# Performance work log

Hardware: AMD Instinct MI355X
Metric: run time of the kernel (lower is better)

The kernel has to match this reference:

```python
import jax, jax.numpy as jnp
import numpy as np

N_NODES = 100000
E_RAW = 3200000
IN_CH = 256
HID = 128
OUT = 64
N_LAYERS = 4


def setup_inputs() -> dict:
    rng = np.random.default_rng(0)
    src = rng.integers(0, N_NODES, E_RAW)
    dst = rng.integers(0, N_NODES, E_RAW)
    # drop self loops (add_self_loops appends them explicitly) and dedupe so the
    # edge list is coalesced (torch sparse .pow acts on coalesced values)
    code = src.astype(np.int64) * N_NODES + dst.astype(np.int64)
    code = np.unique(code[src != dst])
    edge_index = jnp.asarray(np.stack([code // N_NODES, code % N_NODES]), dtype=jnp.int32)

    key = jax.random.key(0)
    ks = jax.random.split(key, 6)
    stdv = 1.0 / np.sqrt(HID)
    x = jax.random.normal(ks[0], (N_NODES, IN_CH), jnp.float32)
    W_lin1 = jax.random.uniform(ks[1], (IN_CH, HID), jnp.float32, -stdv, stdv)
    b_lin1 = jnp.zeros((HID,), jnp.float32)
    W1 = jax.random.uniform(ks[2], (N_LAYERS, HID, HID), jnp.float32, -stdv, stdv)
    W2 = jax.random.uniform(ks[3], (N_LAYERS, HID, HID), jnp.float32, -stdv, stdv)
    W_lin2 = jax.random.uniform(ks[4], (HID, OUT), jnp.float32, -stdv, stdv)
    b_lin2 = jnp.zeros((OUT,), jnp.float32)
    return {"x": x, "W_lin1": W_lin1, "b_lin1": b_lin1, "W1": W1, "W2": W2,
            "W_lin2": W_lin2, "b_lin2": b_lin2, "edge_index": edge_index}


def reference(x, W_lin1, b_lin1, W1, W2, W_lin2, b_lin2, edge_index):
    n = N_NODES
    diag = jnp.arange(n, dtype=edge_index.dtype)
    # add self loops (appended last, so diagonal entries are the final n slots)
    row = jnp.concatenate([edge_index[0], diag])
    col = jnp.concatenate([edge_index[1], diag])
    deg = jax.ops.segment_sum(jnp.ones_like(row, jnp.float32), row, num_segments=n)
    inv_deg_row = 1.0 / deg[row]                     # per-edge 1/deg(src)
    a_vals = inv_deg_row                             # A_rw = D^{-1} A (incl. self loops)
    l_vals = (-inv_deg_row).at[-n:].add(1.0)         # L_rw = I - D^{-1} A (coalesced)

    def spmm(vals, X):
        return jax.ops.segment_sum(vals[:, None] * X[col], row, num_segments=n)

    h = jax.nn.relu(x @ W_lin1 + b_lin1)
    acc = jnp.zeros((n, HID), h.dtype)
    for l in range(N_LAYERS):
        o1 = h @ W1[l]
        o2 = h @ W2[l]
        if l != 0:
            # torch sparse .pow(l) = elementwise power of nonzero values
            o1 = spmm(l_vals ** l, o1)
            o2 = spmm(a_vals ** l, o2)
        if l != N_LAYERS - 1:
            o1 = spmm(a_vals, o1)
            o2 = spmm(l_vals, o2)
        acc = acc + jax.nn.relu(o1) + jax.nn.relu(o2)
    xm = acc / (2 * N_LAYERS)
    return xm @ W_lin2 + b_lin2
```

## Files before the change

kernel.cpp:

```cpp
#include <hip/hip_runtime.h>
#include <hip/hip_bf16.h>
#include <stdint.h>

#define NN   100000
#define ICH  256
#define HID  128
#define OUTF 64

typedef float  f32x4  __attribute__((ext_vector_type(4)));
typedef __bf16 bf16x8 __attribute__((ext_vector_type(8)));

__device__ __forceinline__ float bf2f(uint16_t u){
  union { uint32_t i; float f; } v; v.i = ((uint32_t)u) << 16; return v.f;
}
__device__ __forceinline__ uint16_t f2bf(float f){
  union { float f; uint32_t i; } v; v.f = f;
  uint32_t i = v.i;
  return (uint16_t)((i + 0x7FFFu + ((i >> 16) & 1u)) >> 16);
}
__device__ __forceinline__ uint32_t pack2(float a, float b){
  return (uint32_t)f2bf(a) | ((uint32_t)f2bf(b) << 16);
}

__global__ void k_csr(const int* __restrict__ row, int E, int n,
                      int* __restrict__ rp, float* __restrict__ r){
  int i = blockIdx.x * blockDim.x + threadIdx.x;
  if (i > n) return;
  int lo = 0, hi = E;
  while (lo < hi){
    int mid = (lo + hi) >> 1;
    if (row[mid] < i) lo = mid + 1; else hi = mid;
  }
  rp[i] = lo;
  if (i < n){
    int lo2 = lo, hi2 = E;
    while (lo2 < hi2){
      int mid = (lo2 + hi2) >> 1;
      if (row[mid] < i + 1) lo2 = mid + 1; else hi2 = mid;
    }
    r[i] = 1.0f / (float)(lo2 - lo + 1);
  }
}

__global__ void k_wprep(const float* __restrict__ W1, const float* __restrict__ W2,
                        const float* __restrict__ Wl1, const float* __restrict__ Wl2,
                        uint16_t* __restrict__ W1T, uint16_t* __restrict__ W2T,
                        uint16_t* __restrict__ Wl1T, uint16_t* __restrict__ Wl2T){
  int idx = blockIdx.x * blockDim.x + threadIdx.x;
  if (idx < 4 * 128 * 128){
    int l = idx >> 14, rem = idx & 16383, n = rem >> 7, k = rem & 127;
    W1T[idx] = f2bf(W1[l * 16384 + k * 128 + n]);
    W2T[idx] = f2bf(W2[l * 16384 + k * 128 + n]);
  }
  if (idx < 128 * 256){
    int n = idx >> 8, k = idx & 255;
    Wl1T[idx] = f2bf(Wl1[k * 128 + n]);
  }
  if (idx < 64 * 128){
    int n = idx >> 7, k = idx & 127;
    Wl2T[idx] = f2bf(Wl2[k * 64 + n]);
  }
}

__launch_bounds__(256)
__global__ void k_lin1m(const float* __restrict__ x, const uint16_t* __restrict__ Wl1T,
                        const float* __restrict__ b, uint16_t* __restrict__ h){
  __shared__ __align__(16) uint16_t Xs[64][264];
  const int tid = threadIdx.x;
  const int node0 = blockIdx.x * 64;
  const int wv = tid >> 6, lane = tid & 63, lr = lane & 15, lg = lane >> 4;

  #pragma unroll
  for (int i = 0; i < 16; ++i){
    int fi = tid + i * 256;
    int rrow = fi >> 6, c4 = (fi & 63) * 4;
    int nd = node0 + rrow;
    float4 f = (nd < NN) ? *(const float4*)(x + (size_t)nd * ICH + c4)
                         : make_float4(0.f, 0.f, 0.f, 0.f);
    *(uint2*)&Xs[rrow][c4] = make_uint2(pack2(f.x, f.y), pack2(f.z, f.w));
  }
  __syncthreads();

  bf16x8 bfr[2][8];
  #pragma unroll
  for (int n2 = 0; n2 < 2; ++n2){
    const int n = (2 * wv + n2) * 16 + lr;
    const uint16_t* bp = Wl1T + (size_t)n * 256 + lg * 8;
    #pragma unroll
    for (int ks = 0; ks < 8; ++ks)
      bfr[n2][ks] = __builtin_bit_cast(bf16x8, *(const uint4*)(bp + ks * 32));
  }
  float bias[2] = {b[(2 * wv + 0) * 16 + lr], b[(2 * wv + 1) * 16 + lr]};

  #pragma unroll
  for (int rt = 0; rt < 4; ++rt){
    const int row = rt * 16 + lr;
    bf16x8 af[8];
    #pragma unroll
    for (int ks = 0; ks < 8; ++ks)
      af[ks] = __builtin_bit_cast(bf16x8, *(const uint4*)&Xs[row][ks * 32 + lg * 8]);
    #pragma unroll
    for (int n2 = 0; n2 < 2; ++n2){
      f32x4 d = (f32x4){0.f, 0.f, 0.f, 0.f};
      #pragma unroll
      for (int ks = 0; ks < 8; ++ks)
        d = __builtin_amdgcn_mfma_f32_16x16x32_bf16(af[ks], bfr[n2][ks], d, 0, 0, 0);
      const int ncol = (2 * wv + n2) * 16 + lr;
      #pragma unroll
      for (int q = 0; q < 4; ++q){
        int nd = node0 + rt * 16 + lg * 4 + q;
        if (nd < NN){
          float v = d[q] + bias[n2];
          h[(size_t)nd * HID + ncol] = f2bf(v > 0.f ? v : 0.f);
        }
      }
    }
  }
}

__launch_bounds__(256)
__global__ void k_spmmA(const int* __restrict__ col, const int* __restrict__ rp,
                        const float* __restrict__ r, const uint32_t* __restrict__ h,
                        uint32_t* __restrict__ P, uint32_t* __restrict__ T1,
                        uint32_t* __restrict__ T2){
  int wid  = (blockIdx.x * blockDim.x + threadIdx.x) >> 6;
  int lane = threadIdx.x & 63;
  if (wid >= NN) return;
  int e0 = rp[wid], e1 = rp[wid + 1];
  float a0 = 0, b0 = 0, a1 = 0, b1 = 0, a2 = 0, b2 = 0;
  for (int base = e0; base < e1; base += 64){
    int tot = e1 - base;
    int cnt = tot < 64 ? tot : 64;
    int jv  = (lane < cnt) ? col[base + lane] : 0;
    int rvb = (lane < cnt) ? __builtin_bit_cast(int, r[jv]) : 0;
    int k = 0;
    for (; k + 16 <= cnt; k += 16){
      uint32_t hv[16];
      #pragma unroll
      for (int t = 0; t < 16; ++t){
        int j = __builtin_amdgcn_readlane(jv, k + t);
        hv[t] = h[((uint32_t)j << 6) + lane];
      }
      #pragma unroll
      for (int t = 0; t < 16; ++t){
        float rj = __builtin_bit_cast(float, __builtin_amdgcn_readlane(rvb, k + t));
        float r2 = rj * rj;
        float x0 = __builtin_bit_cast(float, hv[t] << 16);
        float x1 = __builtin_bit_cast(float, hv[t] & 0xFFFF0000u);
        a0 += x0;               b0 += x1;
        a1 = fmaf(rj, x0, a1);  b1 = fmaf(rj, x1, b1);
        a2 = fmaf(r2, x0, a2);  b2 = fmaf(r2, x1, b2);
      }
    }
    for (; k + 4 <= cnt; k += 4){
      uint32_t hv[4];
      #pragma unroll
      for (int t = 0; t < 4; ++t){
        int j = __builtin_amdgcn_readlane(jv, k + t);
        hv[t] = h[((uint32_t)j << 6) + lane];
      }
      #pragma unroll
      for (int t = 0; t < 4; ++t){
        float rj = __builtin_bit_cast(float, __builtin_amdgcn_readlane(rvb, k + t));
        float r2 = rj * rj;
        float x0 = __builtin_bit_cast(float, hv[t] << 16);
        float x1 = __builtin_bit_cast(float, hv[t] & 0xFFFF0000u);
        a0 += x0;               b0 += x1;
        a1 = fmaf(rj, x0, a1);  b1 = fmaf(rj, x1, b1);
        a2 = fmaf(r2, x0, a2);  b2 = fmaf(r2, x1, b2);
      }
    }
    for (; k < cnt; ++k){
      int j = __builtin_amdgcn_readlane(jv, k);
      float rj = __builtin_bit_cast(float, __builtin_amdgcn_readlane(rvb, k));
      float r2 = rj * rj;
      uint32_t hv = h[((uint32_t)j << 6) + lane];
      float x0 = __builtin_bit_cast(float, hv << 16);
      float x1 = __builtin_bit_cast(float, hv & 0xFFFF0000u);
      a0 += x0;               b0 += x1;
      a1 = fmaf(rj, x0, a1);  b1 = fmaf(rj, x1, b1);
      a2 = fmaf(r2, x0, a2);  b2 = fmaf(r2, x1, b2);
    }
  }
  size_t o = (size_t)wid * 64 + lane;
  P[o]  = pack2(a0, b0);
  T1[o] = pack2(a1, b1);
  T2[o] = pack2(a2, b2);
}

__launch_bounds__(256)
__global__ void k_spmmB(const int* __restrict__ col, const int* __restrict__ rp,
                        const float* __restrict__ r, const uint32_t* __restrict__ Pm,
                        uint32_t* __restrict__ Q1, uint32_t* __restrict__ Q2){
  int wid  = (blockIdx.x * blockDim.x + threadIdx.x) >> 6;
  int lane = threadIdx.x & 63;
  if (wid >= NN) return;
  int e0 = rp[wid], e1 = rp[wid + 1];
  float a1 = 0, b1 = 0, a2 = 0, b2 = 0;
  for (int base = e0; base < e1; base += 64){
    int tot = e1 - base;
    int cnt = tot < 64 ? tot : 64;
    int jv  = (lane < cnt) ? col[base + lane] : 0;
    int rvb = (lane < cnt) ? __builtin_bit_cast(int, r[jv]) : 0;
    int k = 0;
    for (; k + 16 <= cnt; k += 16){
      uint32_t pv[16];
      #pragma unroll
      for (int t = 0; t < 16; ++t){
        int j = __builtin_amdgcn_readlane(jv, k + t);
        pv[t] = Pm[((uint32_t)j << 6) + lane];
      }
      #pragma unroll
      for (int t = 0; t < 16; ++t){
        float rj = __builtin_bit_cast(float, __builtin_amdgcn_readlane(rvb, k + t));
        float r2 = rj * rj;
        float x0 = __builtin_bit_cast(float, pv[t] << 16);
        float x1 = __builtin_bit_cast(float, pv[t] & 0xFFFF0000u);
        a1 = fmaf(rj, x0, a1);  b1 = fmaf(rj, x1, b1);
        a2 = fmaf(r2, x0, a2);  b2 = fmaf(r2, x1, b2);
      }
    }
    for (; k + 4 <= cnt; k += 4){
      uint32_t pv[4];
      #pragma unroll
      for (int t = 0; t < 4; ++t){
        int j = __builtin_amdgcn_readlane(jv, k + t);
        pv[t] = Pm[((uint32_t)j << 6) + lane];
      }
      #pragma unroll
      for (int t = 0; t < 4; ++t){
        float rj = __builtin_bit_cast(float, __builtin_amdgcn_readlane(rvb, k + t));
        float r2 = rj * rj;
        float x0 = __builtin_bit_cast(float, pv[t] << 16);
        float x1 = __builtin_bit_cast(float, pv[t] & 0xFFFF0000u);
        a1 = fmaf(rj, x0, a1);  b1 = fmaf(rj, x1, b1);
        a2 = fmaf(r2, x0, a2);  b2 = fmaf(r2, x1, b2);
      }
    }
    for (; k < cnt; ++k){
      int j = __builtin_amdgcn_readlane(jv, k);
      float rj = __builtin_bit_cast(float, __builtin_amdgcn_readlane(rvb, k));
      float r2 = rj * rj;
      uint32_t pv = Pm[((uint32_t)j << 6) + lane];
      float x0 = __builtin_bit_cast(float, pv << 16);
      float x1 = __builtin_bit_cast(float, pv & 0xFFFF0000u);
      a1 = fmaf(rj, x0, a1);  b1 = fmaf(rj, x1, b1);
      a2 = fmaf(r2, x0, a2);  b2 = fmaf(r2, x1, b2);
    }
  }
  size_t o = (size_t)wid * 64 + lane;
  Q1[o] = pack2(a1, b1);
  Q2[o] = pack2(a2, b2);
}

__launch_bounds__(512)
__global__ void k_epi5(const uint32_t* __restrict__ h,  const uint32_t* __restrict__ P,
                       const uint32_t* __restrict__ T1, const uint32_t* __restrict__ T2,
                       const uint32_t* __restrict__ Q1, const uint32_t* __restrict__ Q2,
                       const float* __restrict__ r,
                       const uint16_t* __restrict__ W1T, const uint16_t* __restrict__ W2T,
                       const uint16_t* __restrict__ Wl2T, const float* __restrict__ b2,
                       float* __restrict__ out){
  __shared__ __align__(16) uint32_t Mu[2][64][68];
  const int tid = threadIdx.x;
  const int node0 = blockIdx.x * 64;
  const int wv = tid >> 6, lane = tid & 63, lr = lane & 15, lg = lane >> 4;

  const int nb = tid >> 3;
  const int qc = tid & 7;
  const int nd = node0 + nb;
  const int rn = nd < NN ? nd : NN - 1;
  const float rv = r[rn];
  const size_t ub = (size_t)rn * 64;
  const int cc2[2] = {qc, qc + 8};

  f32x4 acc[4];
  #pragma unroll
  for (int rt = 0; rt < 4; ++rt) acc[rt] = (f32x4){0.f, 0.f, 0.f, 0.f};

  auto mfma_phase = [&](const uint16_t* Wa, const uint16_t* Wb){
    #pragma unroll
    for (int m = 0; m < 2; ++m){
      const uint16_t* bp = (m ? Wb : Wa) + (size_t)(wv * 16 + lr) * 128 + lg * 8;
      bf16x8 bfr[4];
      #pragma unroll
      for (int ks = 0; ks < 4; ++ks)
        bfr[ks] = __builtin_bit_cast(bf16x8, *(const uint4*)(bp + ks * 32));
      #pragma unroll
      for (int rt = 0; rt < 4; ++rt){
        const int row = rt * 16 + lr;
        f32x4 d = (f32x4){0.f, 0.f, 0.f, 0.f};
        #pragma unroll
        for (int ks = 0; ks < 4; ++ks){
          bf16x8 af = __builtin_bit_cast(bf16x8, *(const uint4*)&Mu[m][row][ks * 16 + lg * 4]);
          d = __builtin_amdgcn_mfma_f32_16x16x32_bf16(af, bfr[ks], d, 0, 0, 0);
        }
        #pragma unroll
        for (int q = 0; q < 4; ++q)
          acc[rt][q] += (d[q] > 0.f ? d[q] : 0.f);
      }
    }
  };

  uint4 vh[2], vP[2], vT1[2], vQ1[2];
  #pragma unroll
  for (int ci = 0; ci < 2; ++ci){
    vh[ci]  = *(const uint4*)(h  + ub + cc2[ci] * 4);
    vP[ci]  = *(const uint4*)(P  + ub + cc2[ci] * 4);
    vT1[ci] = *(const uint4*)(T1 + ub + cc2[ci] * 4);
    vQ1[ci] = *(const uint4*)(Q1 + ub + cc2[ci] * 4);
  }

  #pragma unroll
  for (int ci = 0; ci < 2; ++ci){
    const uint32_t* ah = (const uint32_t*)&vh[ci];
    const uint32_t* ap = (const uint32_t*)&vP[ci];
    uint32_t o1[4], o2[4];
    #pragma unroll
    for (int w = 0; w < 4; ++w){
      float m1s[2], m2s[2];
      #pragma unroll
      for (int s = 0; s < 2; ++s){
        float hh = bf2f((uint16_t)(s ? (ah[w] >> 16) : ah[w]));
        float pp = bf2f((uint16_t)(s ? (ap[w] >> 16) : ap[w]));
        float F = rv * (pp + hh);
        m1s[s] = F; m2s[s] = hh - F;
      }
      o1[w] = pack2(m1s[0], m1s[1]);
      o2[w] = pack2(m2s[0], m2s[1]);
    }
    *(uint4*)&Mu[0][nb][cc2[ci] * 4] = make_uint4(o1[0], o1[1], o1[2], o1[3]);
    *(uint4*)&Mu[1][nb][cc2[ci] * 4] = make_uint4(o2[0], o2[1], o2[2], o2[3]);
  }
  __syncthreads();
  mfma_phase(W1T, W2T);
  __syncthreads();

  #pragma unroll
  for (int ci = 0; ci < 2; ++ci){
    const uint32_t* ah = (const uint32_t*)&vh[ci];
    const uint32_t* ap = (const uint32_t*)&vP[ci];
    const uint32_t* at = (const uint32_t*)&vT1[ci];
    const uint32_t* aq = (const uint32_t*)&vQ1[ci];
    uint32_t o1[4], o2[4];
    #pragma unroll
    for (int w = 0; w < 4; ++w){
      float m1s[2], m2s[2];
      #pragma unroll
      for (int s = 0; s < 2; ++s){
        float hh = bf2f((uint16_t)(s ? (ah[w] >> 16) : ah[w]));
        float pp = bf2f((uint16_t)(s ? (ap[w] >> 16) : ap[w]));
        float t1 = bf2f((uint16_t)(s ? (at[w] >> 16) : at[w]));
        float q1 = bf2f((uint16_t)(s ? (aq[w] >> 16) : aq[w]));
        float F = rv * (pp + hh);
        float G = hh - F;
        m1s[s] = rv * (pp - q1 - t1 + G);
        m2s[s] = F - rv * (q1 + t1 + F);
      }
      o1[w] = pack2(m1s[0], m1s[1]);
      o2[w] = pack2(m2s[0], m2s[1]);
    }
    *(uint4*)&Mu[0][nb][cc2[ci] * 4] = make_uint4(o1[0], o1[1], o1[2], o1[3]);
    *(uint4*)&Mu[1][nb][cc2[ci] * 4] = make_uint4(o2[0], o2[1], o2[2], o2[3]);
  }
  uint4 vT2[2], vQ2[2];
  #pragma unroll
  for (int ci = 0; ci < 2; ++ci){
    vT2[ci] = *(const uint4*)(T2 + ub + cc2[ci] * 4);
    vQ2[ci] = *(const uint4*)(Q2 + ub + cc2[ci] * 4);
  }
  __syncthreads();
  mfma_phase(W1T + 16384, W2T + 16384);
  __syncthreads();

  #pragma unroll
  for (int ci = 0; ci < 2; ++ci){
    const uint32_t* ah = (const uint32_t*)&vh[ci];
    const uint32_t* ap = (const uint32_t*)&vP[ci];
    const uint32_t* at1 = (const uint32_t*)&vT1[ci];
    const uint32_t* at2 = (const uint32_t*)&vT2[ci];
    const uint32_t* aq2 = (const uint32_t*)&vQ2[ci];
    uint32_t o1[4], o2[4];
    #pragma unroll
    for (int w = 0; w < 4; ++w){
      float m1s[2], m2s[2];
      #pragma unroll
      for (int s = 0; s < 2; ++s){
        float hh = bf2f((uint16_t)(s ? (ah[w] >> 16) : ah[w]));
        float pp = bf2f((uint16_t)(s ? (ap[w] >> 16) : ap[w]));
        float t1 = bf2f((uint16_t)(s ? (at1[w] >> 16) : at1[w]));
        float t2 = bf2f((uint16_t)(s ? (at2[w] >> 16) : at2[w]));
        float q2 = bf2f((uint16_t)(s ? (aq2[w] >> 16) : aq2[w]));
        float omr = 1.f - rv;
        float G2 = rv * rv * pp + omr * omr * hh;
        m1s[s] = rv * (q2 + pp - 2.f * t1 + t2 + G2);
        float F2 = rv * rv * (pp + hh);
        m2s[s] = F2 - rv * (q2 + t2 + F2);
      }
      o1[w] = pack2(m1s[0], m1s[1]);
      o2[w] = pack2(m2s[0], m2s[1]);
    }
    *(uint4*)&Mu[0][nb][cc2[ci] * 4] = make_uint4(o1[0], o1[1], o1[2], o1[3]);
    *(uint4*)&Mu[1][nb][cc2[ci] * 4] = make_uint4(o2[0], o2[1], o2[2], o2[3]);
  }
  __syncthreads();
  mfma_phase(W1T + 2 * 16384, W2T + 2 * 16384);
  __syncthreads();

  #pragma unroll
  for (int ci = 0; ci < 2; ++ci){
    const uint32_t* ah = (const uint32_t*)&vh[ci];
    const uint32_t* ap = (const uint32_t*)&vP[ci];
    uint32_t o1[4], o2[4];
    #pragma unroll
    for (int w = 0; w < 4; ++w){
      float m1s[2], m2s[2];
      #pragma unroll
      for (int s = 0; s < 2; ++s){
        float hh = bf2f((uint16_t)(s ? (ah[w] >> 16) : ah[w]));
        float pp = bf2f((uint16_t)(s ? (ap[w] >> 16) : ap[w]));
        float omr = 1.f - rv;
        float r3 = rv * rv * rv;
        m1s[s] = omr * omr * omr * hh - r3 * pp;
        m2s[s] = r3 * (pp + hh);
      }
      o1[w] = pack2(m1s[0], m1s[1]);
      o2[w] = pack2(m2s[0], m2s[1]);
    }
    *(uint4*)&Mu[0][nb][cc2[ci] * 4] = make_uint4(o1[0], o1[1], o1[2], o1[3]);
    *(uint4*)&Mu[1][nb][cc2[ci] * 4] = make_uint4(o2[0], o2[1], o2[2], o2[3]);
  }
  __syncthreads();
  mfma_phase(W1T + 3 * 16384, W2T + 3 * 16384);
  __syncthreads();

  uint16_t* Mb = (uint16_t*)&Mu[0][0][0];
  #pragma unroll
  for (int rt = 0; rt < 4; ++rt)
    #pragma unroll
    for (int q = 0; q < 4; ++q){
      int row = rt * 16 + lg * 4 + q;
      int colb = wv * 16 + lr;
      Mb[row * 136 + colb] = f2bf(acc[rt][q] * 0.125f);
    }
  __syncthreads();

  const int rt2 = wv >> 1;
  const int arow = rt2 * 16 + lr;
  bf16x8 af2[4];
  #pragma unroll
  for (int ks = 0; ks < 4; ++ks)
    af2[ks] = __builtin_bit_cast(bf16x8, *(const uint4*)&Mu[0][arow][ks * 16 + lg * 4]);
  #pragma unroll
  for (int ntl = 0; ntl < 2; ++ntl){
    const int nt = (wv & 1) * 2 + ntl;
    f32x4 d = (f32x4){0.f, 0.f, 0.f, 0.f};
    #pragma unroll
    for (int ks = 0; ks < 4; ++ks){
      bf16x8 bfr = __builtin_bit_cast(bf16x8,
          *(const uint4*)(Wl2T + (size_t)(nt * 16 + lr) * 128 + ks * 32 + lg * 8));
      d = __builtin_amdgcn_mfma_f32_16x16x32_bf16(af2[ks], bfr, d, 0, 0, 0);
    }
    float bias = b2[nt * 16 + lr];
    #pragma unroll
    for (int q = 0; q < 4; ++q){
      int rr = node0 + rt2 * 16 + lg * 4 + q;
      if (rr < NN) out[(size_t)rr * OUTF + nt * 16 + lr] = d[q] + bias;
    }
  }
}

extern "C" void kernel_launch(void* const* d_in, const int* in_sizes, int n_in,
                              void* d_out, int out_size, void* d_ws, size_t ws_size,
                              hipStream_t stream){
  const float* x   = (const float*)d_in[0];
  const float* Wl1 = (const float*)d_in[1];
  const float* bl1 = (const float*)d_in[2];
  const float* W1  = (const float*)d_in[3];
  const float* W2  = (const float*)d_in[4];
  const float* Wl2 = (const float*)d_in[5];
  const float* bl2 = (const float*)d_in[6];
  const int*   ei  = (const int*)d_in[7];
  int E = in_sizes[7] / 2;
  const int* rowp = ei;
  const int* colp = ei + E;

  char* ws = (char*)d_ws;
  size_t off = 0;
  auto alloc = [&](size_t bytes) -> void* {
    void* p = ws + off;
    off += (bytes + 255) & ~(size_t)255;
    return p;
  };
  const size_t MATB = (size_t)NN * HID * 2;
  uint32_t* h  = (uint32_t*)alloc(MATB);
  uint32_t* P  = (uint32_t*)alloc(MATB);
  uint32_t* T1 = (uint32_t*)alloc(MATB);
  uint32_t* T2 = (uint32_t*)alloc(MATB);
  uint32_t* Q1 = (uint32_t*)alloc(MATB);
  uint32_t* Q2 = (uint32_t*)alloc(MATB);
  float* r  = (float*)alloc((size_t)NN * 4);
  int* rp   = (int*)alloc((size_t)(NN + 1) * 4);
  uint16_t* W1T  = (uint16_t*)alloc((size_t)4 * 128 * 128 * 2);
  uint16_t* W2T  = (uint16_t*)alloc((size_t)4 * 128 * 128 * 2);
  uint16_t* Wl1T = (uint16_t*)alloc((size_t)128 * 256 * 2);
  uint16_t* Wl2T = (uint16_t*)alloc((size_t)64 * 128 * 2);

  k_wprep<<<(4 * 128 * 128 + 255) / 256, 256, 0, stream>>>(W1, W2, Wl1, Wl2,
                                                           W1T, W2T, Wl1T, Wl2T);
  k_csr<<<(NN + 1 + 255) / 256, 256, 0, stream>>>(rowp, E, NN, rp, r);
  k_lin1m<<<(NN + 63) / 64, 256, 0, stream>>>(x, Wl1T, bl1, (uint16_t*)h);
  k_spmmA<<<(NN + 3) / 4, 256, 0, stream>>>(colp, rp, r, h, P, T1, T2);
  k_spmmB<<<(NN + 3) / 4, 256, 0, stream>>>(colp, rp, r, P, Q1, Q2);
  k_epi5<<<(NN + 63) / 64, 512, 0, stream>>>(h, P, T1, T2, Q1, Q2, r,
                                             W1T, W2T, Wl2T, bl2, (float*)d_out);
}
```

Before: 403.1 us.

## Software-pipeline neighbor gathers in SpMM and double-buffer LDS in epilogue

Both SpMM kernels now prefetch the next 16 neighbor rows into a second register array while accumulating the current 16. This keeps more gather loads in flight and hides latency on the memory-bound irregular reads. The epilogue kernel double-buffers its shared-memory staging tiles, which removes one __syncthreads per layer, and raises wave priority around the MFMA phases so matrix work and staging can overlap. The trade-off is higher register use in the SpMM kernels, which may lower occupancy, and twice the LDS in the epilogue.

After: 408.5 us. Within noise of the previous version (+1.3%).

```diff
diff --git a/kernel.cpp b/kernel.cpp
--- a/kernel.cpp
+++ b/kernel.cpp
@@ -134,23 +134,44 @@
     int jv  = (lane < cnt) ? col[base + lane] : 0;
     int rvb = (lane < cnt) ? __builtin_bit_cast(int, r[jv]) : 0;
     int k = 0;
-    for (; k + 16 <= cnt; k += 16){
-      uint32_t hv[16];
+    if (cnt >= 16){
+      uint32_t A[16], B[16];
       #pragma unroll
       for (int t = 0; t < 16; ++t){
-        int j = __builtin_amdgcn_readlane(jv, k + t);
-        hv[t] = h[((uint32_t)j << 6) + lane];
+        int j = __builtin_amdgcn_readlane(jv, t);
+        A[t] = h[((uint32_t)j << 6) + lane];
+      }
+      while (k + 32 <= cnt){
+        #pragma unroll
+        for (int t = 0; t < 16; ++t){
+          int j = __builtin_amdgcn_readlane(jv, k + 16 + t);
+          B[t] = h[((uint32_t)j << 6) + lane];
+        }
+        #pragma unroll
+        for (int t = 0; t < 16; ++t){
+          float rj = __builtin_bit_cast(float, __builtin_amdgcn_readlane(rvb, k + t));
+          float r2 = rj * rj;
+          float x0 = __builtin_bit_cast(float, A[t] << 16);
+          float x1 = __builtin_bit_cast(float, A[t] & 0xFFFF0000u);
+          a0 += x0;               b0 += x1;
+          a1 = fmaf(rj, x0, a1);  b1 = fmaf(rj, x1, b1);
+          a2 = fmaf(r2, x0, a2);  b2 = fmaf(r2, x1, b2);
+        }
+        #pragma unroll
+        for (int t = 0; t < 16; ++t) A[t] = B[t];
+        k += 16;
       }
       #pragma unroll
       for (int t = 0; t < 16; ++t){
         float rj = __builtin_bit_cast(float, __builtin_amdgcn_readlane(rvb, k + t));
         float r2 = rj * rj;
-        float x0 = __builtin_bit_cast(float, hv[t] << 16);
-        float x1 = __builtin_bit_cast(float, hv[t] & 0xFFFF0000u);
+        float x0 = __builtin_bit_cast(float, A[t] << 16);
+        float x1 = __builtin_bit_cast(float, A[t] & 0xFFFF0000u);
         a0 += x0;               b0 += x1;
         a1 = fmaf(rj, x0, a1);  b1 = fmaf(rj, x1, b1);
         a2 = fmaf(r2, x0, a2);  b2 = fmaf(r2, x1, b2);
       }
+      k += 16;
     }
     for (; k + 4 <= cnt; k += 4){
       uint32_t hv[4];
@@ -203,22 +224,42 @@
     int jv  = (lane < cnt) ? col[base + lane] : 0;
     int rvb = (lane < cnt) ? __builtin_bit_cast(int, r[jv]) : 0;
     int k = 0;
-    for (; k + 16 <= cnt; k += 16){
-      uint32_t pv[16];
+    if (cnt >= 16){
+      uint32_t A[16], B[16];
       #pragma unroll
       for (int t = 0; t < 16; ++t){
-        int j = __builtin_amdgcn_readlane(jv, k + t);
-        pv[t] = Pm[((uint32_t)j << 6) + lane];
+        int j = __builtin_amdgcn_readlane(jv, t);
+        A[t] = Pm[((uint32_t)j << 6) + lane];
+      }
+      while (k + 32 <= cnt){
+        #pragma unroll
+        for (int t = 0; t < 16; ++t){
+          int j = __builtin_amdgcn_readlane(jv, k + 16 + t);
+          B[t] = Pm[((uint32_t)j << 6) + lane];
+        }
+        #pragma unroll
+        for (int t = 0; t < 16; ++t){
+          float rj = __builtin_bit_cast(float, __builtin_amdgcn_readlane(rvb, k + t));
+          float r2 = rj * rj;
+          float x0 = __builtin_bit_cast(float, A[t] << 16);
+          float x1 = __builtin_bit_cast(float, A[t] & 0xFFFF0000u);
+          a1 = fmaf(rj, x0, a1);  b1 = fmaf(rj, x1, b1);
+          a2 = fmaf(r2, x0, a2);  b2 = fmaf(r2, x1, b2);
+        }
+        #pragma unroll
+        for (int t = 0; t < 16; ++t) A[t] = B[t];
+        k += 16;
       }
       #pragma unroll
       for (int t = 0; t < 16; ++t){
         float rj = __builtin_bit_cast(float, __builtin_amdgcn_readlane(rvb, k + t));
         float r2 = rj * rj;
-        float x0 = __builtin_bit_cast(float, pv[t] << 16);
-        float x1 = __builtin_bit_cast(float, pv[t] & 0xFFFF0000u);
+        float x0 = __builtin_bit_cast(float, A[t] << 16);
+        float x1 = __builtin_bit_cast(float, A[t] & 0xFFFF0000u);
         a1 = fmaf(rj, x0, a1);  b1 = fmaf(rj, x1, b1);
         a2 = fmaf(r2, x0, a2);  b2 = fmaf(r2, x1, b2);
       }
+      k += 16;
     }
     for (; k + 4 <= cnt; k += 4){
       uint32_t pv[4];
@@ -254,14 +295,14 @@
 }
 
 __launch_bounds__(512)
-__global__ void k_epi5(const uint32_t* __restrict__ h,  const uint32_t* __restrict__ P,
+__global__ void k_epi8(const uint32_t* __restrict__ h,  const uint32_t* __restrict__ P,
                        const uint32_t* __restrict__ T1, const uint32_t* __restrict__ T2,
                        const uint32_t* __restrict__ Q1, const uint32_t* __restrict__ Q2,
                        const float* __restrict__ r,
                        const uint16_t* __restrict__ W1T, const uint16_t* __restrict__ W2T,
                        const uint16_t* __restrict__ Wl2T, const float* __restrict__ b2,
                        float* __restrict__ out){
-  __shared__ __align__(16) uint32_t Mu[2][64][68];
+  __shared__ __align__(16) uint32_t Mu[2][2][64][68];
   const int tid = threadIdx.x;
   const int node0 = blockIdx.x * 64;
   const int wv = tid >> 6, lane = tid & 63, lr = lane & 15, lg = lane >> 4;
@@ -278,7 +319,8 @@
   #pragma unroll
   for (int rt = 0; rt < 4; ++rt) acc[rt] = (f32x4){0.f, 0.f, 0.f, 0.f};
 
-  auto mfma_phase = [&](const uint16_t* Wa, const uint16_t* Wb){
+  auto mfma_phase = [&](int buf, const uint16_t* Wa, const uint16_t* Wb){
+    __builtin_amdgcn_s_setprio(1);
     #pragma unroll
     for (int m = 0; m < 2; ++m){
       const uint16_t* bp = (m ? Wb : Wa) + (size_t)(wv * 16 + lr) * 128 + lg * 8;
@@ -292,7 +334,8 @@
         f32x4 d = (f32x4){0.f, 0.f, 0.f, 0.f};
         #pragma unroll
         for (int ks = 0; ks < 4; ++ks){
-          bf16x8 af = __builtin_bit_cast(bf16x8, *(const uint4*)&Mu[m][row][ks * 16 + lg * 4]);
+          bf16x8 af = __builtin_bit_cast(bf16x8,
+              *(const uint4*)&Mu[buf][m][row][ks * 16 + lg * 4]);
           d = __builtin_amdgcn_mfma_f32_16x16x32_bf16(af, bfr[ks], d, 0, 0, 0);
         }
         #pragma unroll
@@ -300,6 +343,7 @@
           acc[rt][q] += (d[q] > 0.f ? d[q] : 0.f);
       }
     }
+    __builtin_amdgcn_s_setprio(0);
   };
 
   uint4 vh[2], vP[2], vT1[2], vQ1[2];
@@ -329,13 +373,12 @@
       o1[w] = pack2(m1s[0], m1s[1]);
       o2[w] = pack2(m2s[0], m2s[1]);
     }
-    *(uint4*)&Mu[0][nb][cc2[ci] * 4] = make_uint4(o1[0], o1[1], o1[2], o1[3]);
-    *(uint4*)&Mu[1][nb][cc2[ci] * 4] = make_uint4(o2[0], o2[1], o2[2], o2[3]);
+    *(uint4*)&Mu[0][0][nb][cc2[ci] * 4] = make_uint4(o1[0], o1[1], o1[2], o1[3]);
+    *(uint4*)&Mu[0][1][nb][cc2[ci] * 4] = make_uint4(o2[0], o2[1], o2[2], o2[3]);
   }
   __syncthreads();
-  mfma_phase(W1T, W2T);
-  __syncthreads();
-
+
+  mfma_phase(0, W1T, W2T);
   #pragma unroll
   for (int ci = 0; ci < 2; ++ci){
     const uint32_t* ah = (const uint32_t*)&vh[ci];
@@ -360,8 +403,8 @@
       o1[w] = pack2(m1s[0], m1s[1]);
       o2[w] = pack2(m2s[0], m2s[1]);
     }
-    *(uint4*)&Mu[0][nb][cc2[ci] * 4] = make_uint4(o1[0], o1[1], o1[2], o1[3]);
-    *(uint4*)&Mu[1][nb][cc2[ci] * 4] = make_uint4(o2[0], o2[1], o2[2], o2[3]);
+    *(uint4*)&Mu[1][0][nb][cc2[ci] * 4] = make_uint4(o1[0], o1[1], o1[2], o1[3]);
+    *(uint4*)&Mu[1][1][nb][cc2[ci] * 4] = make_uint4(o2[0], o2[1], o2[2], o2[3]);
   }
   uint4 vT2[2], vQ2[2];
   #pragma unroll
@@ -370,9 +413,8 @@
     vQ2[ci] = *(const uint4*)(Q2 + ub + cc2[ci] * 4);
   }
   __syncthreads();
-  mfma_phase(W1T + 16384, W2T + 16384);
-  __syncthreads();
-
+
+  mfma_phase(1, W1T + 16384, W2T + 16384);
   #pragma unroll
   for (int ci = 0; ci < 2; ++ci){
     const uint32_t* ah = (const uint32_t*)&vh[ci];
@@ -400,13 +442,12 @@
       o1[w] = pack2(m1s[0], m1s[1]);
       o2[w] = pack2(m2s[0], m2s[1]);
     }
-    *(uint4*)&Mu[0][nb][cc2[ci] * 4] = make_uint4(o1[0], o1[1], o1[2], o1[3]);
-    *(uint4*)&Mu[1][nb][cc2[ci] * 4] = make_uint4(o2[0], o2[1], o2[2], o2[3]);
+    *(uint4*)&Mu[0][0][nb][cc2[ci] * 4] = make_uint4(o1[0], o1[1], o1[2], o1[3]);
+    *(uint4*)&Mu[0][1][nb][cc2[ci] * 4] = make_uint4(o2[0], o2[1], o2[2], o2[3]);
   }
   __syncthreads();
-  mfma_phase(W1T + 2 * 16384, W2T + 2 * 16384);
-  __syncthreads();
-
+
+  mfma_phase(0, W1T + 2 * 16384, W2T + 2 * 16384);
   #pragma unroll
   for (int ci = 0; ci < 2; ++ci){
     const uint32_t* ah = (const uint32_t*)&vh[ci];
@@ -427,14 +468,14 @@
       o1[w] = pack2(m1s[0], m1s[1]);
       o2[w] = pack2(m2s[0], m2s[1]);
     }
-    *(uint4*)&Mu[0][nb][cc2[ci] * 4] = make_uint4(o1[0], o1[1], o1[2], o1[3]);
-    *(uint4*)&Mu[1][nb][cc2[ci] * 4] = make_uint4(o2[0], o2[1], o2[2], o2[3]);
+    *(uint4*)&Mu[1][0][nb][cc2[ci] * 4] = make_uint4(o1[0], o1[1], o1[2], o1[3]);
+    *(uint4*)&Mu[1][1][nb][cc2[ci] * 4] = make_uint4(o2[0], o2[1], o2[2], o2[3]);
   }
   __syncthreads();
-  mfma_phase(W1T + 3 * 16384, W2T + 3 * 16384);
-  __syncthreads();
-
-  uint16_t* Mb = (uint16_t*)&Mu[0][0][0];
+
+  mfma_phase(1, W1T + 3 * 16384, W2T + 3 * 16384);
+
+  uint16_t* Mb = (uint16_t*)&Mu[0][0][0][0];
   #pragma unroll
   for (int rt = 0; rt < 4; ++rt)
     #pragma unroll
@@ -450,7 +491,7 @@
   bf16x8 af2[4];
   #pragma unroll
   for (int ks = 0; ks < 4; ++ks)
-    af2[ks] = __builtin_bit_cast(bf16x8, *(const uint4*)&Mu[0][arow][ks * 16 + lg * 4]);
+    af2[ks] = __builtin_bit_cast(bf16x8, *(const uint4*)&Mu[0][0][arow][ks * 16 + lg * 4]);
   #pragma unroll
   for (int ntl = 0; ntl < 2; ++ntl){
     const int nt = (wv & 1) * 2 + ntl;
@@ -512,6 +553,6 @@
   k_lin1m<<<(NN + 63) / 64, 256, 0, stream>>>(x, Wl1T, bl1, (uint16_t*)h);
   k_spmmA<<<(NN + 3) / 4, 256, 0, stream>>>(colp, rp, r, h, P, T1, T2);
   k_spmmB<<<(NN + 3) / 4, 256, 0, stream>>>(colp, rp, r, P, Q1, Q2);
-  k_epi5<<<(NN + 63) / 64, 512, 0, stream>>>(h, P, T1, T2, Q1, Q2, r,
+  k_epi8<<<(NN + 63) / 64, 512, 0, stream>>>(h, P, T1, T2, Q1, Q2, r,
                                              W1T, W2T, Wl2T, bl2, (float*)d_out);
 }
```
